# Kernel tuning notes

Hardware: AMD Instinct MI355X
Metric: run time of the kernel (lower is better)

The kernel has to match this reference:

```python
import jax, jax.numpy as jnp
import numpy as np

HID = 64
NUM_LAYERS = 4
IN_DIM = 1
OUT_DIM = 1
LN_EPS = 1e-5


def setup_inputs() -> dict:
    key = jax.random.key(0)
    ks = jax.random.split(key, 2 * NUM_LAYERS + 5)
    B, S = 1024, 512
    inp = {"x": jax.random.normal(ks[0], (B, S, IN_DIM), dtype=jnp.float32)}
    # per-layer gate weights, stored as [in+H, 4H] (x @ W + b, equivalent to torch Linear)
    for l in range(NUM_LAYERS):
        in_dim = IN_DIM if l == 0 else HID
        fan_in = in_dim + HID
        bound = 1.0 / np.sqrt(fan_in)
        inp[f"W{l}"] = jax.random.uniform(ks[1 + 2 * l], (fan_in, 4 * HID), jnp.float32, -bound, bound)
        inp[f"b{l}"] = jax.random.uniform(ks[2 + 2 * l], (4 * HID,), jnp.float32, -bound, bound)
    inp["ln_g"] = jnp.ones((HID,), jnp.float32)
    inp["ln_b"] = jnp.zeros((HID,), jnp.float32)
    bo = 1.0 / np.sqrt(HID)
    inp["Wout"] = jax.random.uniform(ks[-2], (HID, OUT_DIM), jnp.float32, -bo, bo)
    inp["bout"] = jax.random.uniform(ks[-1], (OUT_DIM,), jnp.float32, -bo, bo)
    return inp


def _lstm_forward(x, Ws, bs):
    B = x.shape[0]
    h0 = tuple(jnp.zeros((B, HID), x.dtype) for _ in range(NUM_LAYERS))
    c0 = tuple(jnp.zeros((B, HID), x.dtype) for _ in range(NUM_LAYERS))

    def step(carry, xt):
        h, c = carry
        inp = xt
        new_h, new_c = [], []
        for l in range(NUM_LAYERS):
            z = jnp.concatenate([inp, h[l]], axis=-1) @ Ws[l] + bs[l]  # [B, 4H]
            i, f, g, o = jnp.split(z, 4, axis=-1)
            i = jax.nn.sigmoid(i)
            f = jax.nn.sigmoid(f)
            g = jnp.tanh(g)
            o = jax.nn.sigmoid(o)
            c_new = f * c[l] + i * g
            h_new = o * jnp.tanh(c_new)
            new_h.append(h_new)
            new_c.append(c_new)
            inp = h_new
        return (tuple(new_h), tuple(new_c)), new_h[-1]

    xs = jnp.swapaxes(x, 0, 1)  # [S, B, in]
    _, outs = jax.lax.scan(step, (h0, c0), xs)
    return jnp.swapaxes(outs, 0, 1)  # [B, S, H]


def reference(x, W0, b0, W1, b1, W2, b2, W3, b3, ln_g, ln_b, Wout, bout):
    Ws = (W0, W1, W2, W3)
    bs = (b0, b1, b2, b3)
    out = _lstm_forward(x, Ws, bs)  # [B, S, H]
    mu = jnp.mean(out, axis=-1, keepdims=True)
    var = jnp.mean(jnp.square(out - mu), axis=-1, keepdims=True)
    normed = (out - mu) * jax.lax.rsqrt(var + LN_EPS) * ln_g + ln_b
    return normed @ Wout + bout  # [B, S, 1]
```

## Files before the change

kernel.cpp:

```cpp
#include <hip/hip_runtime.h>

#define SEQ   512
#define NTHR  1024
#define NBLK  256

typedef _Float16 f16x8 __attribute__((ext_vector_type(8)));
typedef float    f32x4 __attribute__((ext_vector_type(4)));

#define MFMA(a, b, c) __builtin_amdgcn_mfma_f32_16x16x32_f16((a), (b), (c), 0, 0, 0)

__device__ __forceinline__ float sig_(float x) {
    return __builtin_amdgcn_rcpf(1.0f + __builtin_amdgcn_exp2f(x * -1.4426950408889634f));
}
__device__ __forceinline__ float tanh_(float x) {
    return fmaf(2.0f, __builtin_amdgcn_rcpf(1.0f + __builtin_amdgcn_exp2f(x * -2.8853900817779268f)), -1.0f);
}

#define TICK(P0,P1,P2,P3, Q0,Q1,Q2,Q3, RD, WR, TAU)                            \
    {                                                                          \
        const int tB = (TAU) - 2 * ell;                                        \
        const bool actB = (unsigned)tB < (unsigned)SEQ;                        \
        const bool actA = (unsigned)(tB + 1) < (unsigned)SEQ;                  \
        if (actB) {                             \
            const f16x8 b2 = *(const f16x8*)(hb + (RD) + sfA0);                \
            const f16x8 b3 = *(const f16x8*)(hb + (RD) + sfA1);                \
            P0 = MFMA(wf[0][2], b2, P0);  P1 = MFMA(wf[1][2], b2, P1);         \
            P2 = MFMA(wf[2][2], b2, P2);  P3 = MFMA(wf[3][2], b2, P3);         \
            P0 = MFMA(wf[0][3], b3, P0);  P1 = MFMA(wf[1][3], b3, P1);         \
            P2 = MFMA(wf[2][3], b3, P2);  P3 = MFMA(wf[3][3], b3, P3);         \
        }                                                                      \
        if (actA) {                  \
            f16x8 b0, b1;                                                      \
            if (ell == 0) {                                                    \
                if (lam == 0) xf[0] = (_Float16)xrow[tB + 1];                  \
                b0 = xf; b1 = xf;                   \
            } else {                                                           \
                b0 = *(const f16x8*)(hb + (RD) + inA0);                        \
                b1 = *(const f16x8*)(hb + (RD) + inA1);                        \
            }                                                                  \
            Q0 = *(const f32x4*)(bldsW + 0);                                   \
            Q1 = *(const f32x4*)(bldsW + 64);                                  \
            Q2 = *(const f32x4*)(bldsW + 128);                                 \
            Q3 = *(const f32x4*)(bldsW + 192);                                 \
            Q0 = MFMA(wf[0][0], b0, Q0);  Q1 = MFMA(wf[1][0], b0, Q1);         \
            Q2 = MFMA(wf[2][0], b0, Q2);  Q3 = MFMA(wf[3][0], b0, Q3);         \
            Q0 = MFMA(wf[0][1], b1, Q0);  Q1 = MFMA(wf[1][1], b1, Q1);         \
            Q2 = MFMA(wf[2][1], b1, Q2);  Q3 = MFMA(wf[3][1], b1, Q3);         \
        }                                                                      \
        if (actB) {                 \
            const f32x4 s01 = k1b ? P1 : P0;                                   \
            const f32x4 s23 = k1b ? P3 : P2;                                   \
            const f32x4 aK  = k2b ? s23 : s01;                                 \
            const float gi = sig_(aK[0]);                                      \
            const float gf = sig_(aK[1]);                                      \
            const float gg = tanh_(aK[2]);                                     \
            const float go = sig_(aK[3]);                                      \
            cstK = fmaf(gf, cstK, gi * gg);                                    \
            const float hn = go * tanh_(cstK);                                 \
            *(_Float16*)(hb + (WR) + wrKS) = (_Float16)hn;                     \
            if (ell == 3) {                                                    \
                float v1 = hn, v2 = hn * hn, v3 = hn * gwK;                    \
                v1 += __shfl_xor(v1, 4, 64);  v2 += __shfl_xor(v2, 4, 64);  v3 += __shfl_xor(v3, 4, 64);  \
                v1 += __shfl_xor(v1, 8, 64);  v2 += __shfl_xor(v2, 8, 64);  v3 += __shfl_xor(v3, 8, 64);  \
                v1 += __shfl_xor(v1, 16, 64); v2 += __shfl_xor(v2, 16, 64); v3 += __shfl_xor(v3, 16, 64); \
                v1 += __shfl_xor(v1, 32, 64); v2 += __shfl_xor(v2, 32, 64); v3 += __shfl_xor(v3, 32, 64); \
                if (bc < 4) {                                                  \
                    float* pp = &part[tB & 15][om][bc][0];                     \
                    pp[0] = v1; pp[1] = v2; pp[2] = v3;                        \
                }                                                              \
            }                                                                  \
        }                                                                      \
        __syncthreads();                                                       \
        {                                                                      \
            const int t3 = (TAU) - 6;                                          \
            if (t3 >= 7 && (t3 & 7) == 7) {                                    \
                const int row = tid >> 4, sub = tid & 15;                      \
                if (row < 32) {                                                \
                    const int sl = row >> 2, b = row & 3;                      \
                    const int slot = (t3 - 7 + sl) & 15;                       \
                    float u1 = part[slot][sub & 3][b][0];                      \
                    float u2 = part[slot][sub & 3][b][1];                      \
                    float u3 = part[slot][sub & 3][b][2];                      \
                    u1 += __shfl_xor(u1, 1, 64); u2 += __shfl_xor(u2, 1, 64); u3 += __shfl_xor(u3, 1, 64); \
                    u1 += __shfl_xor(u1, 2, 64); u2 += __shfl_xor(u2, 2, 64); u3 += __shfl_xor(u3, 2, 64); \
                    if (sub == 0) {                                            \
                        const float mu = u1 * (1.0f / 64.0f);                  \
                        float var = fmaf(u2, 1.0f / 64.0f, -mu * mu);          \
                        var = fmaxf(var, 0.0f);                                \
                        const float rs = rsqrtf(var + 1e-5f);                  \
                        out[(bb * 4 + b) * SEQ + (t3 - 7) + sl] =              \
                            fmaf(rs, fmaf(-mu, Sgw, u3), Sbw);                 \
                    }                                                          \
                }                                                              \
            }                                                                  \
        }                                                                      \
    }

__global__ __launch_bounds__(NTHR, 4) void lstm4_swp(
    const float* __restrict__ x,
    const float* __restrict__ W0, const float* __restrict__ B0,
    const float* __restrict__ W1, const float* __restrict__ B1,
    const float* __restrict__ W2, const float* __restrict__ B2,
    const float* __restrict__ W3, const float* __restrict__ B3,
    const float* __restrict__ ln_g, const float* __restrict__ ln_b,
    const float* __restrict__ Wout, const float* __restrict__ bout,
    float* __restrict__ out)
{
    __shared__ __align__(16) _Float16 hbuf[2][4][4][64];
    __shared__ float xall[4][SEQ];
    __shared__ float part[16][4][4][3];
    __shared__ __align__(16) float blds[4][16][4][4];
    __shared__ float sconst[2];

    const int tid  = threadIdx.x;
    const int lane = tid & 63;
    const int w    = tid >> 6;
    const int ell  = w >> 2;
    const int om   = w & 3;
    const int lam  = lane >> 4;
    const int bc   = lane & 15;
    const int br   = bc & 3;
    const int kq   = bc >> 2;
    const int bb   = blockIdx.x;

    for (int i = tid; i < 4 * SEQ; i += NTHR)
        xall[i >> 9][i & 511] = x[bb * 4 * SEQ + i];
    for (int i = tid; i < 2 * 4 * 4 * 64; i += NTHR)
        ((_Float16*)hbuf)[i] = (_Float16)0.0f;
    {
        const int L = tid >> 8, idx = tid & 255;
        const int T = idx >> 4, lm = (idx >> 2) & 3, r = idx & 3;
        const float* Bp4 = (L == 0) ? B0 : (L == 1) ? B1 : (L == 2) ? B2 : B3;
        ((float*)blds)[tid] = Bp4[r * 64 + T * 4 + lm];
    }
    if (tid < 64) {
        float a = ln_g[tid] * Wout[tid];
        float b = ln_b[tid] * Wout[tid];
#pragma unroll
        for (int off = 32; off > 0; off >>= 1) {
            a += __shfl_xor(a, off, 64);
            b += __shfl_xor(b, off, 64);
        }
        if (tid == 0) { sconst[0] = a; sconst[1] = b; }
    }

    const float* Wp = (ell == 0) ? W0 : (ell == 1) ? W1 : (ell == 2) ? W2 : W3;

    f16x8 wf[4][4];
#pragma unroll
    for (int i = 0; i < 4; ++i) {
        const int T  = om * 4 + i;
        const int cA = (bc & 3) * 64 + T * 4 + (bc >> 2);
        if (ell == 0) {
#pragma unroll
            for (int kt = 0; kt < 2; ++kt)
#pragma unroll
                for (int e = 0; e < 8; ++e)
                    wf[i][2 + kt][e] = (_Float16)W0[(1 + kt * 32 + lam * 8 + e) * 256 + cA];
#pragma unroll
            for (int e = 0; e < 8; ++e) { wf[i][0][e] = (_Float16)0.0f; wf[i][1][e] = (_Float16)0.0f; }
            if (lam == 0) wf[i][0][0] = (_Float16)W0[cA];
        } else {
#pragma unroll
            for (int kt = 0; kt < 4; ++kt)
#pragma unroll
                for (int e = 0; e < 8; ++e)
                    wf[i][kt][e] = (_Float16)Wp[(kt * 32 + lam * 8 + e) * 256 + cA];
        }
    }

    const int   mK  = (om * 4 + kq) * 4 + lam;
    const float gwK = ln_g[mK] * Wout[mK];
    const int   wrK = br * 128 + (((mK >> 3) ^ br) * 16) + (mK & 7) * 2;

    const int a0 = br * 128 + ((lam)     ^ br) * 16;
    const int a1 = br * 128 + ((4 + lam) ^ br) * 16;

    const int inA0 = (ell == 0) ? a0 : (ell - 1) * 512 + a0;
    const int inA1 = (ell == 0) ? a1 : (ell - 1) * 512 + a1;
    const int sfA0 = ell * 512 + a0;
    const int sfA1 = ell * 512 + a1;
    const int wrKS = ell * 512 + wrK;
    const char* const bldsW = (const char*)blds + ell * 1024 + om * 256 + lam * 16;
    const float* const xrow = &xall[br][0];

    const bool k1b = (bc & 4) != 0;
    const bool k2b = (bc & 8) != 0;

    f16x8 xf;
#pragma unroll
    for (int e = 0; e < 8; ++e) xf[e] = (_Float16)0.0f;

    float cstK = 0.0f;
    char* const hb = (char*)hbuf;

    f32x4 aA0, aA1, aA2, aA3;
    f32x4 aB0, aB1, aB2, aB3;

    __syncthreads();
    const float Sgw = sconst[0];
    const float Sbw = sconst[1] + bout[0];

    if (ell == 0) {
        if (lam == 0) xf[0] = (_Float16)xrow[0];
        const f16x8 b0 = xf;
        aA0 = *(const f32x4*)(bldsW + 0);
        aA1 = *(const f32x4*)(bldsW + 64);
        aA2 = *(const f32x4*)(bldsW + 128);
        aA3 = *(const f32x4*)(bldsW + 192);
        aA0 = MFMA(wf[0][0], b0, aA0);
        aA1 = MFMA(wf[1][0], b0, aA1);
        aA2 = MFMA(wf[2][0], b0, aA2);
        aA3 = MFMA(wf[3][0], b0, aA3);
    }

    for (int j = 0; j < 259; ++j) {
        const int tau = 2 * j;
        TICK(aA0, aA1, aA2, aA3, aB0, aB1, aB2, aB3, 2048, 0, tau)
        TICK(aB0, aB1, aB2, aB3, aA0, aA1, aA2, aA3, 0, 2048, tau + 1)
    }
}

extern "C" void kernel_launch(void* const* d_in, const int* in_sizes, int n_in,
                              void* d_out, int out_size, void* d_ws, size_t ws_size,
                              hipStream_t stream)
{
    const float* x    = (const float*)d_in[0];
    const float* W0   = (const float*)d_in[1];
    const float* B0   = (const float*)d_in[2];
    const float* W1   = (const float*)d_in[3];
    const float* B1   = (const float*)d_in[4];
    const float* W2   = (const float*)d_in[5];
    const float* B2   = (const float*)d_in[6];
    const float* W3   = (const float*)d_in[7];
    const float* B3   = (const float*)d_in[8];
    const float* ln_g = (const float*)d_in[9];
    const float* ln_b = (const float*)d_in[10];
    const float* Wout = (const float*)d_in[11];
    const float* bout = (const float*)d_in[12];
    float* out = (float*)d_out;

    lstm4_swp<<<NBLK, NTHR, 0, stream>>>(x, W0, B0, W1, B1, W2, B2, W3, B3,
                                         ln_g, ln_b, Wout, bout, out);
}
```

Measured before the change: 549.2 us.

## Defer layernorm reductions to batched combine and peel boundary pipeline ticks

The last-layer warps no longer run a 4-step, three-value shuffle reduction on every tick. They store raw fp16 h values into a shared ring buffer, and the batched combine step (every 8 ticks) now does the mean, variance and Wout dot products over the 64 hidden units with 512 threads. The main loop is also split into prologue, steady-state and epilogue ranges so the steady state skips the per-tick activity bounds checks. The LN statistics now come from fp16-rounded h values, which changes numerics slightly.

```diff
diff --git a/kernel.cpp b/kernel.cpp
--- a/kernel.cpp
+++ b/kernel.cpp
@@ -5,6 +5,7 @@
 #define NBLK  256
 
 typedef _Float16 f16x8 __attribute__((ext_vector_type(8)));
+typedef _Float16 f16x4 __attribute__((ext_vector_type(4)));
 typedef float    f32x4 __attribute__((ext_vector_type(4)));
 
 #define MFMA(a, b, c) __builtin_amdgcn_mfma_f32_16x16x32_f16((a), (b), (c), 0, 0, 0)
@@ -16,11 +17,11 @@
     return fmaf(2.0f, __builtin_amdgcn_rcpf(1.0f + __builtin_amdgcn_exp2f(x * -2.8853900817779268f)), -1.0f);
 }
 
-#define TICK(P0,P1,P2,P3, Q0,Q1,Q2,Q3, RD, WR, TAU)                            \
+#define TICK(P0,P1,P2,P3, Q0,Q1,Q2,Q3, RD, WR, TAU, CHECKED)                   \
     {                                                                          \
         const int tB = (TAU) - 2 * ell;                                        \
-        const bool actB = (unsigned)tB < (unsigned)SEQ;                        \
-        const bool actA = (unsigned)(tB + 1) < (unsigned)SEQ;                  \
+        const bool actB = !(CHECKED) || ((unsigned)tB < (unsigned)SEQ);        \
+        const bool actA = !(CHECKED) || ((unsigned)(tB + 1) < (unsigned)SEQ);  \
         if (actB) {                             \
             const f16x8 b2 = *(const f16x8*)(hb + (RD) + sfA0);                \
             const f16x8 b3 = *(const f16x8*)(hb + (RD) + sfA1);                \
@@ -58,45 +59,46 @@
             cstK = fmaf(gf, cstK, gi * gg);                                    \
             const float hn = go * tanh_(cstK);                                 \
             *(_Float16*)(hb + (WR) + wrKS) = (_Float16)hn;                     \
-            if (ell == 3) {                                                    \
-                float v1 = hn, v2 = hn * hn, v3 = hn * gwK;                    \
-                v1 += __shfl_xor(v1, 4, 64);  v2 += __shfl_xor(v2, 4, 64);  v3 += __shfl_xor(v3, 4, 64);  \
-                v1 += __shfl_xor(v1, 8, 64);  v2 += __shfl_xor(v2, 8, 64);  v3 += __shfl_xor(v3, 8, 64);  \
-                v1 += __shfl_xor(v1, 16, 64); v2 += __shfl_xor(v2, 16, 64); v3 += __shfl_xor(v3, 16, 64); \
-                v1 += __shfl_xor(v1, 32, 64); v2 += __shfl_xor(v2, 32, 64); v3 += __shfl_xor(v3, 32, 64); \
-                if (bc < 4) {                                                  \
-                    float* pp = &part[tB & 15][om][bc][0];                     \
-                    pp[0] = v1; pp[1] = v2; pp[2] = v3;                        \
-                }                                                              \
-            }                                                                  \
+            if (ell == 3)           \
+                *(_Float16*)((char*)parth + ((tB & 15) << 9) + wrP) = (_Float16)hn; \
         }                                                                      \
         __syncthreads();                                                       \
         {                                                                      \
             const int t3 = (TAU) - 6;                                          \
-            if (t3 >= 7 && (t3 & 7) == 7) {                                    \
-                const int row = tid >> 4, sub = tid & 15;                      \
-                if (row < 32) {                                                \
-                    const int sl = row >> 2, b = row & 3;                      \
-                    const int slot = (t3 - 7 + sl) & 15;                       \
-                    float u1 = part[slot][sub & 3][b][0];                      \
-                    float u2 = part[slot][sub & 3][b][1];                      \
-                    float u3 = part[slot][sub & 3][b][2];                      \
-                    u1 += __shfl_xor(u1, 1, 64); u2 += __shfl_xor(u2, 1, 64); u3 += __shfl_xor(u3, 1, 64); \
-                    u1 += __shfl_xor(u1, 2, 64); u2 += __shfl_xor(u2, 2, 64); u3 += __shfl_xor(u3, 2, 64); \
-                    if (sub == 0) {                                            \
-                        const float mu = u1 * (1.0f / 64.0f);                  \
-                        float var = fmaf(u2, 1.0f / 64.0f, -mu * mu);          \
-                        var = fmaxf(var, 0.0f);                                \
-                        const float rs = rsqrtf(var + 1e-5f);                  \
-                        out[(bb * 4 + b) * SEQ + (t3 - 7) + sl] =              \
-                            fmaf(rs, fmaf(-mu, Sgw, u3), Sbw);                 \
-                    }                                                          \
-                }                                                              \
+            if (t3 >= 7 && (t3 & 7) == 7) COMBINE(t3)                          \
+        }                                                                      \
+    }
+
+#define COMBINE(T3)                                                            \
+    {                                                                          \
+        if (tid < 512) {                                                       \
+            const int row = tid >> 4, sub = tid & 15;                          \
+            const int sl = row >> 2, b = row & 3;                              \
+            const int slot = ((T3) - 7 + sl) & 15;                             \
+            const int m0 = sub * 4;                                            \
+            const f16x4 h4 = *(const f16x4*)&parth[slot][b][m0];               \
+            const f32x4 g4 = *(const f32x4*)&gwlds[m0];                        \
+            const float h0 = (float)h4[0], h1 = (float)h4[1];                  \
+            const float h2 = (float)h4[2], h3 = (float)h4[3];                  \
+            float u1 = (h0 + h1) + (h2 + h3);                                  \
+            float u2 = fmaf(h0, h0, fmaf(h1, h1, fmaf(h2, h2, h3 * h3)));      \
+            float u3 = fmaf(h0, g4[0], fmaf(h1, g4[1], fmaf(h2, g4[2], h3 * g4[3]))); \
+            u1 += __shfl_xor(u1, 1, 64); u2 += __shfl_xor(u2, 1, 64); u3 += __shfl_xor(u3, 1, 64); \
+            u1 += __shfl_xor(u1, 2, 64); u2 += __shfl_xor(u2, 2, 64); u3 += __shfl_xor(u3, 2, 64); \
+            u1 += __shfl_xor(u1, 4, 64); u2 += __shfl_xor(u2, 4, 64); u3 += __shfl_xor(u3, 4, 64); \
+            u1 += __shfl_xor(u1, 8, 64); u2 += __shfl_xor(u2, 8, 64); u3 += __shfl_xor(u3, 8, 64); \
+            if (sub == 0) {                                                    \
+                const float mu = u1 * (1.0f / 64.0f);                          \
+                float var = fmaf(u2, 1.0f / 64.0f, -mu * mu);                  \
+                var = fmaxf(var, 0.0f);                                        \
+                const float rs = rsqrtf(var + 1e-5f);                          \
+                out[(bb * 4 + b) * SEQ + ((T3) - 7) + sl] =                    \
+                    fmaf(rs, fmaf(-mu, Sgw, u3), Sbw);                         \
             }                                                                  \
         }                                                                      \
     }
 
-__global__ __launch_bounds__(NTHR, 4) void lstm4_swp(
+__global__ __launch_bounds__(NTHR, 4) void lstm4_swp2(
     const float* __restrict__ x,
     const float* __restrict__ W0, const float* __restrict__ B0,
     const float* __restrict__ W1, const float* __restrict__ B1,
@@ -108,8 +110,9 @@
 {
     __shared__ __align__(16) _Float16 hbuf[2][4][4][64];
     __shared__ float xall[4][SEQ];
-    __shared__ float part[16][4][4][3];
+    __shared__ __align__(16) _Float16 parth[16][4][64];
     __shared__ __align__(16) float blds[4][16][4][4];
+    __shared__ __align__(16) float gwlds[64];
     __shared__ float sconst[2];
 
     const int tid  = threadIdx.x;
@@ -134,14 +137,15 @@
         ((float*)blds)[tid] = Bp4[r * 64 + T * 4 + lm];
     }
     if (tid < 64) {
-        float a = ln_g[tid] * Wout[tid];
-        float b = ln_b[tid] * Wout[tid];
+        const float a = ln_g[tid] * Wout[tid];
+        gwlds[tid] = a;
+        float sa = a, sb = ln_b[tid] * Wout[tid];
 #pragma unroll
         for (int off = 32; off > 0; off >>= 1) {
-            a += __shfl_xor(a, off, 64);
-            b += __shfl_xor(b, off, 64);
+            sa += __shfl_xor(sa, off, 64);
+            sb += __shfl_xor(sb, off, 64);
         }
-        if (tid == 0) { sconst[0] = a; sconst[1] = b; }
+        if (tid == 0) { sconst[0] = sa; sconst[1] = sb; }
     }
 
     const float* Wp = (ell == 0) ? W0 : (ell == 1) ? W1 : (ell == 2) ? W2 : W3;
@@ -169,9 +173,9 @@
         }
     }
 
-    const int   mK  = (om * 4 + kq) * 4 + lam;
-    const float gwK = ln_g[mK] * Wout[mK];
-    const int   wrK = br * 128 + (((mK >> 3) ^ br) * 16) + (mK & 7) * 2;
+    const int mK  = (om * 4 + kq) * 4 + lam;
+    const int wrK = br * 128 + (((mK >> 3) ^ br) * 16) + (mK & 7) * 2;
+    const int wrP = (br * 64 + mK) * 2;
 
     const int a0 = br * 128 + ((lam)     ^ br) * 16;
     const int a1 = br * 128 + ((4 + lam) ^ br) * 16;
@@ -214,10 +218,20 @@
         aA3 = MFMA(wf[3][0], b0, aA3);
     }
 
-    for (int j = 0; j < 259; ++j) {
+    for (int j = 0; j < 3; ++j) {
         const int tau = 2 * j;
-        TICK(aA0, aA1, aA2, aA3, aB0, aB1, aB2, aB3, 2048, 0, tau)
-        TICK(aB0, aB1, aB2, aB3, aA0, aA1, aA2, aA3, 0, 2048, tau + 1)
+        TICK(aA0, aA1, aA2, aA3, aB0, aB1, aB2, aB3, 2048, 0, tau, true)
+        TICK(aB0, aB1, aB2, aB3, aA0, aA1, aA2, aA3, 0, 2048, tau + 1, true)
+    }
+    for (int j = 3; j < 255; ++j) {
+        const int tau = 2 * j;
+        TICK(aA0, aA1, aA2, aA3, aB0, aB1, aB2, aB3, 2048, 0, tau, false)
+        TICK(aB0, aB1, aB2, aB3, aA0, aA1, aA2, aA3, 0, 2048, tau + 1, false)
+    }
+    for (int j = 255; j < 259; ++j) {
+        const int tau = 2 * j;
+        TICK(aA0, aA1, aA2, aA3, aB0, aB1, aB2, aB3, 2048, 0, tau, true)
+        TICK(aB0, aB1, aB2, aB3, aA0, aA1, aA2, aA3, 0, 2048, tau + 1, true)
     }
 }
 
@@ -240,6 +254,6 @@
     const float* bout = (const float*)d_in[12];
     float* out = (float*)d_out;
 
-    lstm4_swp<<<NBLK, NTHR, 0, stream>>>(x, W0, B0, W1, B1, W2, B2, W3, B3,
-                                         ln_g, ln_b, Wout, bout, out);
-}
+    lstm4_swp2<<<NBLK, NTHR, 0, stream>>>(x, W0, B0, W1, B1, W2, B2, W3, B3,
+                                          ln_g, ln_b, Wout, bout, out);
+}
```

Result: faster. 469.6 us (-14.5%).
